# Kernel optimization log

Hardware: AMD Instinct MI355X
Metric: run time of the kernel (lower is better)

The kernel has to match this reference:

```python
import jax, jax.numpy as jnp
import numpy as np

B, S, E, D, H = 32, 4096, 512, 512, 512


def setup_inputs() -> dict:
    key = jax.random.key(0)
    ks = jax.random.split(key, 7)
    scale = 1.0 / np.sqrt(H)
    return {
        "encoder_hiddens": jax.random.normal(ks[0], (B, S, E), dtype=jnp.float32),
        "decoder_hidden": jax.random.normal(ks[1], (B, D), dtype=jnp.float32),
        "W_enc": jax.random.uniform(ks[2], (H, E), jnp.float32, -scale, scale),
        "b_enc": jax.random.uniform(ks[3], (H,), jnp.float32, -scale, scale),
        "W_dec": jax.random.uniform(ks[4], (H, D), jnp.float32, -scale, scale),
        "b_dec": jax.random.uniform(ks[5], (H,), jnp.float32, -scale, scale),
        "v": jax.random.uniform(ks[6], (H,), jnp.float32, -scale, scale),
    }


def reference(encoder_hiddens, decoder_hidden, W_enc, b_enc, W_dec, b_dec, v):
    # Projections (the two small GEMMs of the original per-timestep loop, batched)
    enc_hs = jnp.einsum("bse,he->bsh", encoder_hiddens, W_enc) + b_enc  # [B,S,H]
    dec_h = decoder_hidden @ W_dec.T + b_dec                            # [B,H]

    # Ragged-length detection: the torch loop breaks at the first all-zero
    # projected encoder row; positions at/after that are excluded (cumulative AND).
    nonzero = jnp.any(enc_hs != 0, axis=-1)                             # [B,S]
    valid = jnp.cumprod(nonzero.astype(jnp.int32), axis=1).astype(bool)

    # Additive (Bahdanau) scores: v . tanh(enc_hs + dec_h)
    scores = jnp.einsum("h,bsh->bs", v, jnp.tanh(enc_hs + dec_h[:, None, :]))
    scores = jnp.where(valid, scores, -jnp.inf)
    attn = jax.nn.softmax(scores, axis=1)                               # [B,S]
    attn = jnp.where(valid, attn, 0.0)

    # Weighted sum of encoder states -> context vector [B,1,E]
    return jnp.sum(encoder_hiddens * attn[..., None], axis=1, keepdims=True)
```

## Files before the change

### kernel.cpp

```cpp
#include <hip/hip_runtime.h>
#include <hip/hip_bf16.h>

#define BATCH 32
#define SEQ   4096
#define EDIM  512
#define HDIM  512
#define NCHUNK 64
#define NBLK  (BATCH * NCHUNK)

typedef unsigned short u16;
typedef unsigned int   u32;

typedef __bf16 bf16x8 __attribute__((ext_vector_type(8)));
typedef float  f32x4  __attribute__((ext_vector_type(4)));

__device__ __forceinline__ u16 bf_rne(float x) {
    u32 u = __float_as_uint(x);
    u32 r = (u + 0x7fffu + ((u >> 16) & 1u)) >> 16;
    return (u16)r;
}
__device__ __forceinline__ u32 pack2(u16 lo, u16 hi) {
    return (u32)lo | ((u32)hi << 16);
}
__device__ __forceinline__ float tanh_fast(float x) {
    float e = __builtin_amdgcn_exp2f(x * 2.88539008177793f);
    return 1.0f - 2.0f * __builtin_amdgcn_rcpf(e + 1.0f);
}

__global__ void prep_kernel(const float* __restrict__ W_enc, uint4* __restrict__ wpack,
                            const float* __restrict__ dec, const float* __restrict__ Wd,
                            const float* __restrict__ b_enc, const float* __restrict__ b_dec,
                            float* __restrict__ dec_bias) {
    int bid = blockIdx.x;
    int t = threadIdx.x;
    if (bid < 4096) {
        int wave = t >> 6, lane = t & 63;
        int p = bid * 4 + wave;
        int b = p >> 9, h = p & 511;
        const float4* wr = reinterpret_cast<const float4*>(Wd)  + h * 128;
        const float4* dr = reinterpret_cast<const float4*>(dec) + b * 128;
        float4 w0 = wr[lane * 2], w1 = wr[lane * 2 + 1];
        float4 d0 = dr[lane * 2], d1 = dr[lane * 2 + 1];
        float s = w0.x * d0.x + w0.y * d0.y + w0.z * d0.z + w0.w * d0.w
                + w1.x * d1.x + w1.y * d1.y + w1.z * d1.z + w1.w * d1.w;
#pragma unroll
        for (int m = 1; m < 64; m <<= 1) s += __shfl_xor(s, m, 64);
        if (lane == 0) dec_bias[p] = s + b_dec[h] + b_enc[h];
    } else {
        int id   = (bid - 4096) * 256 + t;
        int nsub = id >> 10;
        int rem  = id & 1023;
        int kc   = rem >> 6;
        int lane = rem & 63;
        int row  = nsub * 16 + (lane & 15);
        int col  = kc * 32 + (lane >> 4) * 8;
        const float* src = W_enc + row * EDIM + col;
        uint4 o;
        o.x = pack2(bf_rne(src[0]), bf_rne(src[1]));
        o.y = pack2(bf_rne(src[2]), bf_rne(src[3]));
        o.z = pack2(bf_rne(src[4]), bf_rne(src[5]));
        o.w = pack2(bf_rne(src[6]), bf_rne(src[7]));
        wpack[id] = o;
    }
}

#define ASTRIDE 520

__global__ __launch_bounds__(512, 4) void fused_kernel(
    const float* __restrict__ X, const uint4* __restrict__ Wp,
    const float* __restrict__ bias, const float* __restrict__ v,
    float* __restrict__ cpart, float* __restrict__ mpart, float* __restrict__ lpart)
{
    __shared__ alignas(16) u16 Abuf[64 * ASTRIDE];
    __shared__ float sred[8][64];
    __shared__ float pbuf[64];

    const int tid  = threadIdx.x;
    const int wave = tid >> 6, lane = tid & 63;
    const int quad = lane >> 4, l15 = lane & 15;
    const int blk  = blockIdx.x;
    const int b    = blk >> 6;
    const long row0 = (long)blk * 64;
    const float4* X4 = reinterpret_cast<const float4*>(X + row0 * EDIM);

    const int r  = tid >> 3;
    const int c8 = tid & 7;

    float4 st[16];
#pragma unroll
    for (int p = 0; p < 8; p++) {
        int piece = p * 8 + c8;
        st[2 * p]     = X4[r * 128 + piece * 2];
        st[2 * p + 1] = X4[r * 128 + piece * 2 + 1];
    }
#pragma unroll
    for (int p = 0; p < 8; p++) {
        int piece = p * 8 + c8;
        uint4 w;
        w.x = pack2(bf_rne(st[2 * p].x),     bf_rne(st[2 * p].y));
        w.y = pack2(bf_rne(st[2 * p].z),     bf_rne(st[2 * p].w));
        w.z = pack2(bf_rne(st[2 * p + 1].x), bf_rne(st[2 * p + 1].y));
        w.w = pack2(bf_rne(st[2 * p + 1].z), bf_rne(st[2 * p + 1].w));
        *reinterpret_cast<uint4*>(&Abuf[r * ASTRIDE + piece * 8]) = w;
    }

    f32x4 acc[4][4] = {};
    uint4 bcur[4];
#pragma unroll
    for (int jj = 0; jj < 4; jj++)
        bcur[jj] = Wp[((wave * 4 + jj) * 16 + 0) * 64 + lane];
    __syncthreads();

#pragma unroll
    for (int ks = 0; ks < 16; ks++) {
        bf16x8 af[4];
#pragma unroll
        for (int i = 0; i < 4; i++)
            af[i] = *reinterpret_cast<const bf16x8*>(
                &Abuf[(i * 16 + l15) * ASTRIDE + ks * 32 + quad * 8]);
#pragma unroll
        for (int jj = 0; jj < 4; jj++) {
            bf16x8 bfr = __builtin_bit_cast(bf16x8, bcur[jj]);
#pragma unroll
            for (int i = 0; i < 4; i++)
                acc[i][jj] = __builtin_amdgcn_mfma_f32_16x16x32_bf16(
                    af[i], bfr, acc[i][jj], 0, 0, 0);
            if (ks < 15)
                bcur[jj] = Wp[((wave * 4 + jj) * 16 + ks + 1) * 64 + lane];
        }
    }

    float hb[4], hv[4];
#pragma unroll
    for (int jj = 0; jj < 4; jj++) {
        int h = wave * 64 + jj * 16 + l15;
        hb[jj] = bias[b * HDIM + h];
        hv[jj] = v[h];
    }
    float s_acc[16];
#pragma unroll
    for (int x = 0; x < 16; x++) s_acc[x] = 0.f;
#pragma unroll
    for (int i = 0; i < 4; i++)
#pragma unroll
        for (int jj = 0; jj < 4; jj++)
#pragma unroll
            for (int rr = 0; rr < 4; rr++)
                s_acc[i * 4 + rr] += hv[jj] * tanh_fast(acc[i][jj][rr] + hb[jj]);

#pragma unroll
    for (int m = 1; m < 16; m <<= 1)
#pragma unroll
        for (int x = 0; x < 16; x++)
            s_acc[x] += __shfl_xor(s_acc[x], m, 16);

    if (l15 == 0) {
#pragma unroll
        for (int x = 0; x < 16; x++) {
            int i = x >> 2, rr = x & 3;
            sred[wave][i * 16 + quad * 4 + rr] = s_acc[x];
        }
    }
    __syncthreads();

    if (tid < 64) {
        float sc = sred[0][tid] + sred[1][tid] + sred[2][tid] + sred[3][tid]
                 + sred[4][tid] + sred[5][tid] + sred[6][tid] + sred[7][tid];
        float mx = sc;
#pragma unroll
        for (int m = 1; m < 64; m <<= 1) mx = fmaxf(mx, __shfl_xor(mx, m, 64));
        float p = __builtin_amdgcn_exp2f((sc - mx) * 1.44269504088896f);
        float l = p;
#pragma unroll
        for (int m = 1; m < 64; m <<= 1) l += __shfl_xor(l, m, 64);
        pbuf[tid] = p;
        if (tid == 0) { mpart[blk] = mx; lpart[blk] = l; }
    }
    __syncthreads();

    const float* Xc = X + row0 * EDIM + tid;
    float a0 = 0.f, a1 = 0.f;
#pragma unroll 2
    for (int s = 0; s < 64; s += 8) {
        float x[8];
#pragma unroll
        for (int k = 0; k < 8; k++) x[k] = Xc[(s + k) * EDIM];
#pragma unroll
        for (int k = 0; k < 8; k += 2) {
            a0 = fmaf(pbuf[s + k],     x[k],     a0);
            a1 = fmaf(pbuf[s + k + 1], x[k + 1], a1);
        }
    }
    cpart[(long)blk * EDIM + tid] = a0 + a1;
}

__global__ __launch_bounds__(256) void combine_k(const float* __restrict__ cpart,
                                                 const float* __restrict__ mpart,
                                                 const float* __restrict__ lpart,
                                                 float* __restrict__ out) {
    __shared__ float wbuf[64];
    __shared__ float linv_s;
    int b = blockIdx.x, t = threadIdx.x;
    if (t < 64) {
        float m = mpart[b * 64 + t];
        float M = m;
#pragma unroll
        for (int k = 1; k < 64; k <<= 1) M = fmaxf(M, __shfl_xor(M, k, 64));
        float w = __builtin_amdgcn_exp2f((m - M) * 1.44269504088896f);
        float lw = lpart[b * 64 + t] * w;
        float L = lw;
#pragma unroll
        for (int k = 1; k < 64; k <<= 1) L += __shfl_xor(L, k, 64);
        wbuf[t] = w;
        if (t == 0) linv_s = 1.0f / L;
    }
    __syncthreads();
    const float2* cp = reinterpret_cast<const float2*>(cpart) + (long)b * 64 * 256 + t;
    float ax = 0.f, ay = 0.f;
#pragma unroll 2
    for (int i = 0; i < 64; i += 8) {
        float2 x[8];
#pragma unroll
        for (int k = 0; k < 8; k++) x[k] = cp[(i + k) * 256];
#pragma unroll
        for (int k = 0; k < 8; k++) {
            float w = wbuf[i + k];
            ax = fmaf(w, x[k].x, ax);
            ay = fmaf(w, x[k].y, ay);
        }
    }
    float inv = linv_s;
    reinterpret_cast<float2*>(out)[b * 256 + t] = make_float2(ax * inv, ay * inv);
}

extern "C" void kernel_launch(void* const* d_in, const int* in_sizes, int n_in,
                              void* d_out, int out_size, void* d_ws, size_t ws_size,
                              hipStream_t stream) {
    const float* X      = (const float*)d_in[0];
    const float* dec    = (const float*)d_in[1];
    const float* W_enc  = (const float*)d_in[2];
    const float* b_enc  = (const float*)d_in[3];
    const float* W_dec  = (const float*)d_in[4];
    const float* b_dec  = (const float*)d_in[5];
    const float* v      = (const float*)d_in[6];
    float* out = (float*)d_out;

    char* ws = (char*)d_ws;
    uint4* wpack    = (uint4*)ws;
    float* dec_bias = (float*)(ws + (512 << 10));
    float* cpart    = (float*)(ws + (576 << 10));
    float* mpart    = (float*)(ws + (576 << 10) + (4096 << 10));
    float* lpart    = (float*)(ws + (576 << 10) + (4104 << 10));

    prep_kernel  <<<4224, 256, 0, stream>>>(W_enc, wpack, dec, W_dec, b_enc, b_dec,
                                            dec_bias);
    fused_kernel <<<NBLK, 512, 0, stream>>>(X, wpack, dec_bias, v, cpart, mpart, lpart);
    combine_k    <<<BATCH, 256, 0, stream>>>(cpart, mpart, lpart, out);
}
```

Measured before the change: 462.4 us.

## Double-buffer A tile in LDS and pipeline X loads with MFMA K-loop

The full 64x512 bf16 A tile in LDS is replaced by a small double-buffered 64-wide K slice (two 64x72 buffers). Each iteration prefetches the next X chunk and the W fragments while MFMAs run on the current slice. The hand-written RNE conversion is swapped for the hardware v_cvt_pk_bf16_f32 instruction. The LDS footprint drops sharply, which may allow more resident blocks, but the kernel now takes a barrier on every K step.

```diff
diff --git a/kernel.cpp b/kernel.cpp
--- a/kernel.cpp
+++ b/kernel.cpp
@@ -14,18 +14,22 @@
 typedef __bf16 bf16x8 __attribute__((ext_vector_type(8)));
 typedef float  f32x4  __attribute__((ext_vector_type(4)));
 
-__device__ __forceinline__ u16 bf_rne(float x) {
-    u32 u = __float_as_uint(x);
-    u32 r = (u + 0x7fffu + ((u >> 16) & 1u)) >> 16;
-    return (u16)r;
-}
-__device__ __forceinline__ u32 pack2(u16 lo, u16 hi) {
-    return (u32)lo | ((u32)hi << 16);
+__device__ __forceinline__ u32 cvtpk(float lo, float hi) {
+    u32 r;
+    asm("v_cvt_pk_bf16_f32 %0, %1, %2" : "=v"(r) : "v"(lo), "v"(hi));
+    return r;
 }
 __device__ __forceinline__ float tanh_fast(float x) {
     float e = __builtin_amdgcn_exp2f(x * 2.88539008177793f);
     return 1.0f - 2.0f * __builtin_amdgcn_rcpf(e + 1.0f);
 }
+
+#define LDS_BARRIER() do {                                   \
+    __builtin_amdgcn_sched_barrier(0);                       \
+    asm volatile("s_waitcnt lgkmcnt(0)" ::: "memory");       \
+    __builtin_amdgcn_s_barrier();                            \
+    __builtin_amdgcn_sched_barrier(0);                       \
+} while (0)
 
 __global__ void prep_kernel(const float* __restrict__ W_enc, uint4* __restrict__ wpack,
                             const float* __restrict__ dec, const float* __restrict__ Wd,
@@ -56,22 +60,22 @@
         int col  = kc * 32 + (lane >> 4) * 8;
         const float* src = W_enc + row * EDIM + col;
         uint4 o;
-        o.x = pack2(bf_rne(src[0]), bf_rne(src[1]));
-        o.y = pack2(bf_rne(src[2]), bf_rne(src[3]));
-        o.z = pack2(bf_rne(src[4]), bf_rne(src[5]));
-        o.w = pack2(bf_rne(src[6]), bf_rne(src[7]));
+        o.x = cvtpk(src[0], src[1]);
+        o.y = cvtpk(src[2], src[3]);
+        o.z = cvtpk(src[4], src[5]);
+        o.w = cvtpk(src[6], src[7]);
         wpack[id] = o;
     }
 }
 
-#define ASTRIDE 520
+#define ST 72
 
 __global__ __launch_bounds__(512, 4) void fused_kernel(
     const float* __restrict__ X, const uint4* __restrict__ Wp,
     const float* __restrict__ bias, const float* __restrict__ v,
     float* __restrict__ cpart, float* __restrict__ mpart, float* __restrict__ lpart)
 {
-    __shared__ alignas(16) u16 Abuf[64 * ASTRIDE];
+    __shared__ alignas(16) u16 Abuf[2][64 * ST];
     __shared__ float sred[8][64];
     __shared__ float pbuf[64];
 
@@ -85,49 +89,78 @@
 
     const int r  = tid >> 3;
     const int c8 = tid & 7;
-
-    float4 st[16];
-#pragma unroll
-    for (int p = 0; p < 8; p++) {
-        int piece = p * 8 + c8;
-        st[2 * p]     = X4[r * 128 + piece * 2];
-        st[2 * p + 1] = X4[r * 128 + piece * 2 + 1];
-    }
-#pragma unroll
-    for (int p = 0; p < 8; p++) {
-        int piece = p * 8 + c8;
+    const float4* Xr = X4 + r * 128 + c8 * 2;
+    u16* Aw0 = &Abuf[0][r * ST + c8 * 8];
+    u16* Aw1 = &Abuf[1][r * ST + c8 * 8];
+
+    float4 a0 = Xr[0], a1 = Xr[1];
+    uint4 bA[4], bB[4];
+#pragma unroll
+    for (int jj = 0; jj < 4; jj++)
+        bA[jj] = Wp[((wave * 4 + jj) * 16 + 0) * 64 + lane];
+    float4 pA = Xr[16], pB = Xr[17];
+    {
         uint4 w;
-        w.x = pack2(bf_rne(st[2 * p].x),     bf_rne(st[2 * p].y));
-        w.y = pack2(bf_rne(st[2 * p].z),     bf_rne(st[2 * p].w));
-        w.z = pack2(bf_rne(st[2 * p + 1].x), bf_rne(st[2 * p + 1].y));
-        w.w = pack2(bf_rne(st[2 * p + 1].z), bf_rne(st[2 * p + 1].w));
-        *reinterpret_cast<uint4*>(&Abuf[r * ASTRIDE + piece * 8]) = w;
-    }
-
+        w.x = cvtpk(a0.x, a0.y);  w.y = cvtpk(a0.z, a0.w);
+        w.z = cvtpk(a1.x, a1.y);  w.w = cvtpk(a1.z, a1.w);
+        *reinterpret_cast<uint4*>(Aw0) = w;
+    }
     f32x4 acc[4][4] = {};
-    uint4 bcur[4];
-#pragma unroll
-    for (int jj = 0; jj < 4; jj++)
-        bcur[jj] = Wp[((wave * 4 + jj) * 16 + 0) * 64 + lane];
-    __syncthreads();
-
-#pragma unroll
-    for (int ks = 0; ks < 16; ks++) {
+    LDS_BARRIER();
+
+#pragma unroll
+    for (int k = 0; k < 8; k++) {
+        const u16* Ab = Abuf[k & 1];
+
+#pragma unroll
+        for (int jj = 0; jj < 4; jj++)
+            bB[jj] = Wp[((wave * 4 + jj) * 16 + (2 * k + 1)) * 64 + lane];
+
         bf16x8 af[4];
 #pragma unroll
         for (int i = 0; i < 4; i++)
             af[i] = *reinterpret_cast<const bf16x8*>(
-                &Abuf[(i * 16 + l15) * ASTRIDE + ks * 32 + quad * 8]);
+                &Ab[(i * 16 + l15) * ST + quad * 8]);
 #pragma unroll
         for (int jj = 0; jj < 4; jj++) {
-            bf16x8 bfr = __builtin_bit_cast(bf16x8, bcur[jj]);
+            bf16x8 bfr = __builtin_bit_cast(bf16x8, bA[jj]);
 #pragma unroll
             for (int i = 0; i < 4; i++)
                 acc[i][jj] = __builtin_amdgcn_mfma_f32_16x16x32_bf16(
                     af[i], bfr, acc[i][jj], 0, 0, 0);
-            if (ks < 15)
-                bcur[jj] = Wp[((wave * 4 + jj) * 16 + ks + 1) * 64 + lane];
-        }
+        }
+
+        uint4 wq;
+        if (k < 7) {
+            wq.x = cvtpk(pA.x, pA.y);  wq.y = cvtpk(pA.z, pA.w);
+            wq.z = cvtpk(pB.x, pB.y);  wq.w = cvtpk(pB.z, pB.w);
+        }
+
+        if (k < 7) {
+#pragma unroll
+            for (int jj = 0; jj < 4; jj++)
+                bA[jj] = Wp[((wave * 4 + jj) * 16 + (2 * k + 2)) * 64 + lane];
+        }
+
+        if (k < 6) { pA = Xr[(k + 2) * 16]; pB = Xr[(k + 2) * 16 + 1]; }
+
+#pragma unroll
+        for (int i = 0; i < 4; i++)
+            af[i] = *reinterpret_cast<const bf16x8*>(
+                &Ab[(i * 16 + l15) * ST + 32 + quad * 8]);
+#pragma unroll
+        for (int jj = 0; jj < 4; jj++) {
+            bf16x8 bfr = __builtin_bit_cast(bf16x8, bB[jj]);
+#pragma unroll
+            for (int i = 0; i < 4; i++)
+                acc[i][jj] = __builtin_amdgcn_mfma_f32_16x16x32_bf16(
+                    af[i], bfr, acc[i][jj], 0, 0, 0);
+        }
+
+        if (k < 7)
+            *reinterpret_cast<uint4*>((k & 1) ? Aw0 : Aw1) = wq;
+
+        if (k < 7) LDS_BARRIER();
     }
 
     float hb[4], hv[4];
@@ -179,19 +212,19 @@
     __syncthreads();
 
     const float* Xc = X + row0 * EDIM + tid;
-    float a0 = 0.f, a1 = 0.f;
+    float a0c = 0.f, a1c = 0.f;
 #pragma unroll 2
     for (int s = 0; s < 64; s += 8) {
         float x[8];
 #pragma unroll
-        for (int k = 0; k < 8; k++) x[k] = Xc[(s + k) * EDIM];
-#pragma unroll
-        for (int k = 0; k < 8; k += 2) {
-            a0 = fmaf(pbuf[s + k],     x[k],     a0);
-            a1 = fmaf(pbuf[s + k + 1], x[k + 1], a1);
-        }
-    }
-    cpart[(long)blk * EDIM + tid] = a0 + a1;
+        for (int kk = 0; kk < 8; kk++) x[kk] = Xc[(s + kk) * EDIM];
+#pragma unroll
+        for (int kk = 0; kk < 8; kk += 2) {
+            a0c = fmaf(pbuf[s + kk],     x[kk],     a0c);
+            a1c = fmaf(pbuf[s + kk + 1], x[kk + 1], a1c);
+        }
+    }
+    cpart[(long)blk * EDIM + tid] = a0c + a1c;
 }
 
 __global__ __launch_bounds__(256) void combine_k(const float* __restrict__ cpart,
```

Result: no change. 458.2 us (-0.9%).
